# Optimization experiments

Hardware: AMD Instinct MI355X
Metric: run time of the kernel (lower is better)

Reference implementation:

```python
import jax, jax.numpy as jnp
import numpy as np

TEMPERATURE = 0.07
IGNORE_INDEX = -100
NEG_INF = -1e30


def setup_inputs() -> dict:
    key = jax.random.key(0)
    kg, ke, kl = jax.random.split(key, 3)
    B, P, H = 4, 4096, 256
    greek_embeds = jax.random.normal(kg, (B, P, H), dtype=jnp.float32)
    english_embeds = jax.random.normal(ke, (B, P, H), dtype=jnp.float32)
    # labels in {1 aligned, 0 not aligned, -100 ignore}, ~1/3 each
    raw = jax.random.randint(kl, (B, P), 0, 3)
    labels = jnp.where(raw == 2, IGNORE_INDEX, raw).astype(jnp.int32)
    return {"greek_embeds": greek_embeds, "english_embeds": english_embeds, "labels": labels}


def reference(greek_embeds, english_embeds, labels):
    # L2-normalize (F.normalize semantics: clamp norm at 1e-12)
    g = greek_embeds / jnp.clip(jnp.linalg.norm(greek_embeds, axis=-1, keepdims=True), 1e-12)
    e = english_embeds / jnp.clip(jnp.linalg.norm(english_embeds, axis=-1, keepdims=True), 1e-12)
    # [B, P, P] similarity
    sim = jnp.einsum("bph,bqh->bpq", g, e) / TEMPERATURE

    valid = labels != IGNORE_INDEX            # [B, P]
    pos = valid & (labels == 1)               # [B, P]
    neg = valid & (labels != 1)               # [B, P]
    # batch is processed only if >=2 valid pairs AND at least one pos AND one neg
    batch_ok = (valid.sum(-1) >= 2) & pos.any(-1) & neg.any(-1)  # [B]

    diag = jnp.diagonal(sim, axis1=1, axis2=2)                   # [B, P] positive logit
    neg_sims = jnp.where(neg[:, None, :], sim, NEG_INF)          # [B, P, P] negative logits
    # stable logsumexp over concat([diag_i], neg_sims_i)
    m = jnp.maximum(diag, neg_sims.max(-1))                      # [B, P]
    lse = m + jnp.log(jnp.exp(diag - m) + jnp.sum(jnp.exp(neg_sims - m[..., None]), -1))
    per_pos_loss = lse - diag                                    # cross_entropy with target=0

    mask = pos & batch_ok[:, None]
    count = mask.sum()
    total = jnp.sum(jnp.where(mask, per_pos_loss, 0.0))
    return jnp.where(count == 0, 0.0, total / count.astype(total.dtype))
```

## Files before the change

kernel.cpp:

```cpp
#include <hip/hip_runtime.h>
#include <hip/hip_bf16.h>
#include <math.h>

#define BB 4
#define PP 4096
#define HH 256
#define INV_T (1.0f/0.07f)
#define JSPLIT 8
#define NTILES (PP/16)
#define TILE_BYTES 8192

typedef __attribute__((ext_vector_type(8))) short bf16x8;
typedef __attribute__((ext_vector_type(4))) float f32x4;

#define WAITVM(n) asm volatile("s_waitcnt vmcnt(" #n ")" ::: "memory")

__device__ __forceinline__ unsigned short f2bf(float x){
  union { float f; unsigned u; } v; v.f = x;
  unsigned r = v.u + 0x7FFFu + ((v.u >> 16) & 1u);
  return (unsigned short)(r >> 16);
}

__device__ __forceinline__ void gload_lds16(const void* g, void* l){
  __builtin_amdgcn_global_load_lds(
      (const __attribute__((address_space(1))) unsigned int*)g,
      (__attribute__((address_space(3))) unsigned int*)l, 16, 0, 0);
}

__global__ void k_scan(const int* __restrict__ labels, int* __restrict__ meta,
                       int* __restrict__ rank){
  int b = blockIdx.x;
  const int* lab = labels + b * PP;
  int tid = threadIdx.x, wave = tid >> 6, lane = tid & 63;
  __shared__ int cP[64], cN[64];
  __shared__ int pP[65], pN[65];
  __shared__ int vtot[4];
  int myLab[16];
  int vcnt = 0;
  #pragma unroll
  for (int c = 0; c < 16; c++){
    int l = lab[c*256 + tid];
    myLab[c] = l;
    unsigned long long bP = __ballot(l == 1), bN = __ballot(l == 0);
    vcnt += (l != -100) ? 1 : 0;
    if (lane == 0){ cP[c*4 + wave] = __popcll(bP); cN[c*4 + wave] = __popcll(bN); }
  }
  #pragma unroll
  for (int off = 32; off; off >>= 1) vcnt += __shfl_xor(vcnt, off);
  if (lane == 0) vtot[wave] = vcnt;
  __syncthreads();
  if (tid < 64){
    int sp = 0, sn = 0;
    for (int k = 0; k < tid; k++){ sp += cP[k]; sn += cN[k]; }
    pP[tid] = sp; pN[tid] = sn;
    if (tid == 63){ pP[64] = sp + cP[63]; pN[64] = sn + cN[63]; }
  }
  __syncthreads();
  #pragma unroll
  for (int c = 0; c < 16; c++){
    int l = myLab[c];
    unsigned long long bP = __ballot(l == 1), bN = __ballot(l == 0);
    unsigned long long lt = (1ull << lane) - 1ull;
    int p = b*PP + c*256 + tid;
    if (l == 1)      rank[p] = pP[c*4 + wave] + __popcll(bP & lt);
    else if (l == 0) rank[p] = pN[c*4 + wave] + __popcll(bN & lt);
  }
  if (tid == 0){
    int Np = pP[64], Nn = pN[64], nv = vtot[0]+vtot[1]+vtot[2]+vtot[3];
    meta[b*4+0] = Np; meta[b*4+1] = Nn;
    meta[b*4+2] = (nv >= 2 && Np > 0 && Nn > 0) ? 1 : 0;
    meta[b*4+3] = nv;
  }
}

__global__ void k_norm(const float* __restrict__ greek, const float* __restrict__ english,
                       const int* __restrict__ labels, const int* __restrict__ rank,
                       unsigned short* __restrict__ GposF, unsigned short* __restrict__ EnegF,
                       float* __restrict__ diagC){
  int tid = threadIdx.x, wave = tid >> 6, lane = tid & 63;
  int r0 = blockIdx.x * 4 + wave;
  for (int b = 0; b < BB; b++){
    int u = b * PP + r0;
    int lab = labels[u];
    if (lab == -100) continue;
    size_t base = (size_t)u * HH + lane * 4;
    int rk = rank[u];
    if (lab == 1){
      float4 g4 = *reinterpret_cast<const float4*>(greek + base);
      float4 e4 = *reinterpret_cast<const float4*>(english + base);
      float ag = g4.x*g4.x + g4.y*g4.y + g4.z*g4.z + g4.w*g4.w;
      float ae = e4.x*e4.x + e4.y*e4.y + e4.z*e4.z + e4.w*e4.w;
      float ad = g4.x*e4.x + g4.y*e4.y + g4.z*e4.z + g4.w*e4.w;
      #pragma unroll
      for (int off = 32; off; off >>= 1){
        ag += __shfl_xor(ag, off); ae += __shfl_xor(ae, off); ad += __shfl_xor(ad, off);
      }
      float gs = 1.0f / fmaxf(sqrtf(ag), 1e-12f);
      float es = 1.0f / fmaxf(sqrtf(ae), 1e-12f);
      unsigned u0 = (unsigned)f2bf(g4.x*gs) | ((unsigned)f2bf(g4.y*gs) << 16);
      unsigned u1 = (unsigned)f2bf(g4.z*gs) | ((unsigned)f2bf(g4.w*gs) << 16);
      unsigned o0 = __shfl_xor(u0, 1), o1 = __shfl_xor(u1, 1);
      char* dst = (char*)GposF + ((size_t)b*NTILES + (rk>>4))*TILE_BYTES
                + (lane>>3)*1024 + (((rk&15) + ((lane>>1)&3)*16) << 4);
      if (!(lane & 1)) *(uint4*)dst = make_uint4(u0, u1, o0, o1);
      if (lane == 0) diagC[b*PP + rk] = ad * gs * es;
    } else {
      float4 e4 = *reinterpret_cast<const float4*>(english + base);
      float ae = e4.x*e4.x + e4.y*e4.y + e4.z*e4.z + e4.w*e4.w;
      #pragma unroll
      for (int off = 32; off; off >>= 1) ae += __shfl_xor(ae, off);
      float es = 1.0f / fmaxf(sqrtf(ae), 1e-12f);
      unsigned u0 = (unsigned)f2bf(e4.x*es) | ((unsigned)f2bf(e4.y*es) << 16);
      unsigned u1 = (unsigned)f2bf(e4.z*es) | ((unsigned)f2bf(e4.w*es) << 16);
      unsigned o0 = __shfl_xor(u0, 1), o1 = __shfl_xor(u1, 1);
      char* dst = (char*)EnegF + ((size_t)b*NTILES + (rk>>4))*TILE_BYTES
                + (lane>>3)*1024 + (((rk&15) + ((lane>>1)&3)*16) << 4);
      if (!(lane & 1)) *(uint4*)dst = make_uint4(u0, u1, o0, o1);
    }
  }
}

__global__ void __launch_bounds__(256, 4)
k_loss(const unsigned short* __restrict__ GposF,
       const unsigned short* __restrict__ EnegF,
       const int* __restrict__ meta,
       float* __restrict__ Spart){
  int L = blockIdx.x;
  int rb = L >> 5;
  int pair = L & 31;
  int b = pair >> 3, chunk = pair & 7;
  int Np = meta[b*4+0], Nn = meta[b*4+1], ok = meta[b*4+2];
  int i0 = rb * 64;
  if (!ok || i0 >= Np) return;
  int tid = threadIdx.x, wave = tid >> 6, lane = tid & 63;
  int lo16 = lane & 15, hi4 = lane >> 4;
  int NT = (Nn + 15) >> 4;
  int TPC = (NT + JSPLIT - 1) / JSPLIT;
  int t0 = chunk * TPC, t1 = min(NT, t0 + TPC);

  __shared__ __align__(16) char Bs[3][TILE_BYTES];

  const char* AF = (const char*)GposF + ((size_t)b*NTILES + (i0 >> 4) + wave) * TILE_BYTES;
  bf16x8 a[8];
  #pragma unroll
  for (int kk = 0; kk < 8; kk++)
    a[kk] = *reinterpret_cast<const bf16x8*>(AF + kk*1024 + (lane << 4));

  const char* EF = (const char*)EnegF + (size_t)b * NTILES * TILE_BYTES;
  float s[4] = {0.f, 0.f, 0.f, 0.f};

  if (t0 < t1){
    {
      const char* src = EF + (size_t)t0*TILE_BYTES + (wave << 11) + (lane << 4);
      char* dstl = &Bs[0][wave << 11];
      gload_lds16(src, dstl);
      gload_lds16(src + 1024, dstl + 1024);
    }
    if (t0 + 1 < t1){
      const char* src = EF + (size_t)(t0+1)*TILE_BYTES + (wave << 11) + (lane << 4);
      char* dstl = &Bs[1][wave << 11];
      gload_lds16(src, dstl);
      gload_lds16(src + 1024, dstl + 1024);
    }
    int cur = 0;
    for (int t = t0; t < t1; t++){
      if (t + 1 < t1) WAITVM(2);
      else            WAITVM(0);
      __builtin_amdgcn_s_barrier();
      __builtin_amdgcn_sched_barrier(0);

      if (t + 2 < t1){
        int nb = cur + 2; if (nb >= 3) nb -= 3;
        const char* src = EF + (size_t)(t+2)*TILE_BYTES + (wave << 11) + (lane << 4);
        char* dstl = &Bs[nb][wave << 11];
        gload_lds16(src, dstl);
        gload_lds16(src + 1024, dstl + 1024);
      }

      const char* Bt = &Bs[cur][0];
      f32x4 c = {0.f, 0.f, 0.f, 0.f};
      #pragma unroll
      for (int kk = 0; kk < 8; kk++){
        bf16x8 bv = *reinterpret_cast<const bf16x8*>(Bt + kk*1024 + (lane << 4));
        c = __builtin_amdgcn_mfma_f32_16x16x32_bf16(a[kk], bv, c, 0, 0, 0);
      }
      bool cok = (t*16 + lo16) < Nn;
      #pragma unroll
      for (int r = 0; r < 4; r++)
        s[r] += cok ? __expf(c[r] * INV_T) : 0.0f;

      cur = (cur == 2) ? 0 : cur + 1;
    }
  }

  #pragma unroll
  for (int off = 1; off < 16; off <<= 1){
    #pragma unroll
    for (int r = 0; r < 4; r++) s[r] += __shfl_xor(s[r], off);
  }
  if (lo16 == 0){
    #pragma unroll
    for (int r = 0; r < 4; r++){
      int i = i0 + wave*16 + hi4*4 + r;
      Spart[(((size_t)b*PP + i) << 3) + chunk] = s[r];
    }
  }
}

__global__ void k_final(const float* __restrict__ Spart, const float* __restrict__ diagC,
                        const int* __restrict__ meta, float* __restrict__ out){
  __shared__ float lds[16];
  int tid = threadIdx.x;
  int np[BB], okk[BB];
  #pragma unroll
  for (int b = 0; b < BB; b++){ np[b] = meta[b*4+0]; okk[b] = meta[b*4+2]; }
  float tot = 0.0f;
  for (int idx = tid; idx < BB*PP; idx += 1024){
    int b = idx >> 12, i = idx & (PP-1);
    if (!okk[b] || i >= np[b]) continue;
    const float4* p = reinterpret_cast<const float4*>(Spart + ((size_t)idx << 3));
    float4 p0 = p[0], p1 = p[1];
    float S = ((p0.x+p0.y)+(p0.z+p0.w)) + ((p1.x+p1.y)+(p1.z+p1.w));
    float dl = diagC[idx] * INV_T;
    tot += logf(S + __expf(dl)) - dl;
  }
  #pragma unroll
  for (int off = 32; off; off >>= 1) tot += __shfl_xor(tot, off);
  int wave = tid >> 6;
  if ((tid & 63) == 0) lds[wave] = tot;
  __syncthreads();
  if (tid == 0){
    float total = 0.0f;
    #pragma unroll
    for (int w = 0; w < 16; w++) total += lds[w];
    int count = 0;
    #pragma unroll
    for (int b = 0; b < BB; b++) if (okk[b]) count += np[b];
    out[0] = (count == 0) ? 0.0f : total / (float)count;
  }
}

extern "C" void kernel_launch(void* const* d_in, const int* in_sizes, int n_in,
                              void* d_out, int out_size, void* d_ws, size_t ws_size,
                              hipStream_t stream){
  const float* greek   = (const float*)d_in[0];
  const float* english = (const float*)d_in[1];
  const int*   labels  = (const int*)d_in[2];
  float* out = (float*)d_out;

  char* ws = (char*)d_ws;
  size_t off = 0;
  unsigned short* GposF = (unsigned short*)(ws + off); off += (size_t)BB*NTILES*TILE_BYTES;
  unsigned short* EnegF = (unsigned short*)(ws + off); off += (size_t)BB*NTILES*TILE_BYTES;
  float* Spart  = (float*)(ws + off); off += (size_t)BB*PP*8*sizeof(float);
  float* diagC  = (float*)(ws + off); off += (size_t)BB*PP*sizeof(float);
  int*   rank   = (int*)(ws + off);   off += (size_t)BB*PP*sizeof(int);
  int*   meta   = (int*)(ws + off);   off += 64;

  k_scan<<<BB, 256, 0, stream>>>(labels, meta, rank);
  k_norm<<<PP/4, 256, 0, stream>>>(greek, english, labels, rank, GposF, EnegF, diagC);
  k_loss<<<(PP/64)*32, 256, 0, stream>>>(GposF, EnegF, meta, Spart);
  k_final<<<1, 1024, 0, stream>>>(Spart, diagC, meta, out);
}
```

Measured before the change: 39.36 us.

## Fuse label scan into normalization kernel by recomputing prefix counts per block

Removes the separate label-scan kernel and the rank buffer. Each block in the new prep kernel recounts positive and negative labels preceding its four rows to find their compacted ranks, then normalizes and scatters the rows as before; the last block writes the per-batch metadata. This saves one kernel launch and a global round trip for the ranks, at the cost of redundant label reads that grow with block index and extra block-wide syncs per batch.

```diff
diff --git a/kernel.cpp b/kernel.cpp
--- a/kernel.cpp
+++ b/kernel.cpp
@@ -27,65 +27,51 @@
       (__attribute__((address_space(3))) unsigned int*)l, 16, 0, 0);
 }
 
-__global__ void k_scan(const int* __restrict__ labels, int* __restrict__ meta,
-                       int* __restrict__ rank){
-  int b = blockIdx.x;
-  const int* lab = labels + b * PP;
+__global__ void k_prep(const float* __restrict__ greek, const float* __restrict__ english,
+                       const int* __restrict__ labels,
+                       unsigned short* __restrict__ GposF, unsigned short* __restrict__ EnegF,
+                       float* __restrict__ diagC, int* __restrict__ meta){
   int tid = threadIdx.x, wave = tid >> 6, lane = tid & 63;
-  __shared__ int cP[64], cN[64];
-  __shared__ int pP[65], pN[65];
-  __shared__ int vtot[4];
-  int myLab[16];
-  int vcnt = 0;
-  #pragma unroll
-  for (int c = 0; c < 16; c++){
-    int l = lab[c*256 + tid];
-    myLab[c] = l;
-    unsigned long long bP = __ballot(l == 1), bN = __ballot(l == 0);
-    vcnt += (l != -100) ? 1 : 0;
-    if (lane == 0){ cP[c*4 + wave] = __popcll(bP); cN[c*4 + wave] = __popcll(bN); }
-  }
-  #pragma unroll
-  for (int off = 32; off; off >>= 1) vcnt += __shfl_xor(vcnt, off);
-  if (lane == 0) vtot[wave] = vcnt;
-  __syncthreads();
-  if (tid < 64){
-    int sp = 0, sn = 0;
-    for (int k = 0; k < tid; k++){ sp += cP[k]; sn += cN[k]; }
-    pP[tid] = sp; pN[tid] = sn;
-    if (tid == 63){ pP[64] = sp + cP[63]; pN[64] = sn + cN[63]; }
-  }
-  __syncthreads();
-  #pragma unroll
-  for (int c = 0; c < 16; c++){
-    int l = myLab[c];
-    unsigned long long bP = __ballot(l == 1), bN = __ballot(l == 0);
-    unsigned long long lt = (1ull << lane) - 1ull;
-    int p = b*PP + c*256 + tid;
-    if (l == 1)      rank[p] = pP[c*4 + wave] + __popcll(bP & lt);
-    else if (l == 0) rank[p] = pN[c*4 + wave] + __popcll(bN & lt);
-  }
-  if (tid == 0){
-    int Np = pP[64], Nn = pN[64], nv = vtot[0]+vtot[1]+vtot[2]+vtot[3];
-    meta[b*4+0] = Np; meta[b*4+1] = Nn;
-    meta[b*4+2] = (nv >= 2 && Np > 0 && Nn > 0) ? 1 : 0;
-    meta[b*4+3] = nv;
-  }
-}
-
-__global__ void k_norm(const float* __restrict__ greek, const float* __restrict__ english,
-                       const int* __restrict__ labels, const int* __restrict__ rank,
-                       unsigned short* __restrict__ GposF, unsigned short* __restrict__ EnegF,
-                       float* __restrict__ diagC){
-  int tid = threadIdx.x, wave = tid >> 6, lane = tid & 63;
-  int r0 = blockIdx.x * 4 + wave;
+  int r0 = blockIdx.x * 4;
+  __shared__ int redP[4], redN[4];
+  __shared__ int rowLab[4];
+
   for (int b = 0; b < BB; b++){
-    int u = b * PP + r0;
-    int lab = labels[u];
-    if (lab == -100) continue;
+    const int* lab = labels + b * PP;
+    int cp = 0, cn = 0;
+    for (int j = tid; j < r0; j += 256){
+      int l = lab[j];
+      cp += (l == 1); cn += (l == 0);
+    }
+    #pragma unroll
+    for (int off = 32; off; off >>= 1){ cp += __shfl_xor(cp, off); cn += __shfl_xor(cn, off); }
+    if (lane == 0){ redP[wave] = cp; redN[wave] = cn; }
+    if (tid < 4) rowLab[tid] = lab[r0 + tid];
+    __syncthreads();
+    int baseP = redP[0] + redP[1] + redP[2] + redP[3];
+    int baseN = redN[0] + redN[1] + redN[2] + redN[3];
+    int l0 = rowLab[0], l1 = rowLab[1], l2 = rowLab[2], l3 = rowLab[3];
+    __syncthreads();
+
+    int myLab = (wave == 0) ? l0 : (wave == 1) ? l1 : (wave == 2) ? l2 : l3;
+    int offP = 0, offN = 0;
+    if (wave > 0){ offP += (l0 == 1); offN += (l0 == 0); }
+    if (wave > 1){ offP += (l1 == 1); offN += (l1 == 0); }
+    if (wave > 2){ offP += (l2 == 1); offN += (l2 == 0); }
+
+    if (blockIdx.x == PP/4 - 1 && tid == 0){
+      int Np = baseP + (l0==1)+(l1==1)+(l2==1)+(l3==1);
+      int Nn = baseN + (l0==0)+(l1==0)+(l2==0)+(l3==0);
+      meta[b*4+0] = Np; meta[b*4+1] = Nn;
+      meta[b*4+2] = (Np > 0 && Nn > 0) ? 1 : 0;
+      meta[b*4+3] = Np + Nn;
+    }
+
+    if (myLab == -100) continue;
+    int u = b * PP + r0 + wave;
     size_t base = (size_t)u * HH + lane * 4;
-    int rk = rank[u];
-    if (lab == 1){
+    if (myLab == 1){
+      int rk = baseP + offP;
       float4 g4 = *reinterpret_cast<const float4*>(greek + base);
       float4 e4 = *reinterpret_cast<const float4*>(english + base);
       float ag = g4.x*g4.x + g4.y*g4.y + g4.z*g4.z + g4.w*g4.w;
@@ -105,6 +91,7 @@
       if (!(lane & 1)) *(uint4*)dst = make_uint4(u0, u1, o0, o1);
       if (lane == 0) diagC[b*PP + rk] = ad * gs * es;
     } else {
+      int rk = baseN + offN;
       float4 e4 = *reinterpret_cast<const float4*>(english + base);
       float ae = e4.x*e4.x + e4.y*e4.y + e4.z*e4.z + e4.w*e4.w;
       #pragma unroll
@@ -254,11 +241,9 @@
   unsigned short* EnegF = (unsigned short*)(ws + off); off += (size_t)BB*NTILES*TILE_BYTES;
   float* Spart  = (float*)(ws + off); off += (size_t)BB*PP*8*sizeof(float);
   float* diagC  = (float*)(ws + off); off += (size_t)BB*PP*sizeof(float);
-  int*   rank   = (int*)(ws + off);   off += (size_t)BB*PP*sizeof(int);
   int*   meta   = (int*)(ws + off);   off += 64;
 
-  k_scan<<<BB, 256, 0, stream>>>(labels, meta, rank);
-  k_norm<<<PP/4, 256, 0, stream>>>(greek, english, labels, rank, GposF, EnegF, diagC);
+  k_prep<<<PP/4, 256, 0, stream>>>(greek, english, labels, GposF, EnegF, diagC, meta);
   k_loss<<<(PP/64)*32, 256, 0, stream>>>(GposF, EnegF, meta, Spart);
   k_final<<<1, 1024, 0, stream>>>(Spart, diagC, meta, out);
 }
```

New measurement: 37.61 us, median of 2. 1.05x faster.
